# Kernel tuning notes

Measured on AMD Instinct MI355X. Metric: run time of the kernel, lower is better.

Reference implementation:

```python
import jax, jax.numpy as jnp
import numpy as np

N_HEADS = 16
HID_DIM = 64
INPUT_DIM = 1024
B, L = 4, 1024
NEG = -10000000000.0


def setup_inputs() -> dict:
    key = jax.random.key(0)
    ks = jax.random.split(key, 10)
    d = INPUT_DIM
    h = N_HEADS * HID_DIM
    s = 1.0 / np.sqrt(d)
    return {
        "query": jax.random.normal(ks[0], (B, L, d), dtype=jnp.float32),
        "key": jax.random.normal(ks[1], (B, L, d), dtype=jnp.float32),
        "value": jax.random.normal(ks[2], (B, L, d), dtype=jnp.float32),
        "mask": jax.random.randint(ks[3], (B, 1, L, L), 0, 2, dtype=jnp.int32),
        "wq": jax.random.normal(ks[4], (d, h), dtype=jnp.float32) * s,
        "bq": jnp.zeros((h,), dtype=jnp.float32),
        "wk": jax.random.normal(ks[5], (d, h), dtype=jnp.float32) * s,
        "bk": jnp.zeros((h,), dtype=jnp.float32),
        "wv": jax.random.normal(ks[6], (d, h), dtype=jnp.float32) * s,
        "bv": jnp.zeros((h,), dtype=jnp.float32),
    }


def _split_heads(x):
    # [B, L, H*D] -> [B, H, L, D]
    b, l, _ = x.shape
    return x.reshape(b, l, N_HEADS, HID_DIM).transpose(0, 2, 1, 3)


def reference(query, key, value, mask, wq, bq, wk, bk, wv, bv):
    scale = jnp.sqrt(jnp.float32(HID_DIM))
    Q = _split_heads(query @ wq + bq)   # [B,H,L,D]
    K = _split_heads(key @ wk + bk)
    V = _split_heads(value @ wv + bv)
    energy = jnp.einsum("bhqd,bhkd->bhqk", Q, K) / scale
    energy = jnp.where(mask == 0, jnp.float32(NEG), energy)
    attention = energy  # NOTE: softmax is intentionally skipped, as in the source
    x = jnp.einsum("bhqk,bhkd->bhqd", attention, V)
    x = x.transpose(0, 2, 1, 3).reshape(query.shape[0], -1, N_HEADS * HID_DIM)
    return (attention, x)
```

## Files before the change

kernel.cpp:

```cpp
#include <hip/hip_runtime.h>
#include <stdint.h>
#include <stddef.h>


typedef __attribute__((ext_vector_type(8))) short short8;
typedef __attribute__((ext_vector_type(4))) float f32x4;
typedef __attribute__((ext_vector_type(4))) int i32x4;
typedef __attribute__((ext_vector_type(2))) unsigned int u32x2;

#define MFMA16(a, b, c) __builtin_amdgcn_mfma_f32_16x16x32_bf16(a, b, c, 0, 0, 0)

using gptr_t = const __attribute__((address_space(1))) void*;
using lptr_t = __attribute__((address_space(3))) void*;

#define NEGV -10000000000.0f
#define NEGV_BF16 0xD015u

__device__ __forceinline__ unsigned short f2bf(float f) {
  uint32_t u = __builtin_bit_cast(uint32_t, f);
  u += 0x7FFFu + ((u >> 16) & 1u);
  return (unsigned short)(u >> 16);
}

__global__ __launch_bounds__(256) void k_convert(
    const float* __restrict__ q, const float* __restrict__ k, const float* __restrict__ v,
    unsigned short* __restrict__ oq, unsigned short* __restrict__ ok,
    unsigned short* __restrict__ ov) {
  const int z = blockIdx.z;
  const float* src = z == 0 ? q : z == 1 ? k : v;
  unsigned short* dst = z == 0 ? oq : z == 1 ? ok : ov;
  const size_t idx = ((size_t)blockIdx.x * 256 + threadIdx.x) * 8;
  f32x4 a = *(const f32x4*)(src + idx);
  f32x4 b = *(const f32x4*)(src + idx + 4);
  short8 o;
  o[0] = (short)f2bf(a[0]); o[1] = (short)f2bf(a[1]);
  o[2] = (short)f2bf(a[2]); o[3] = (short)f2bf(a[3]);
  o[4] = (short)f2bf(b[0]); o[5] = (short)f2bf(b[1]);
  o[6] = (short)f2bf(b[2]); o[7] = (short)f2bf(b[3]);
  *(short8*)(dst + idx) = o;
}

__global__ __launch_bounds__(256) void k_wt(
    const float* __restrict__ wq, const float* __restrict__ wk, const float* __restrict__ wv,
    unsigned short* __restrict__ tq, unsigned short* __restrict__ tk,
    unsigned short* __restrict__ tv) {
  const int z = blockIdx.z;
  const float* src = z == 0 ? wq : z == 1 ? wk : wv;
  unsigned short* dst = z == 0 ? tq : z == 1 ? tk : tv;
  __shared__ unsigned short t[64][65];
  const int n0 = blockIdx.x * 64, k0 = blockIdx.y * 64;
#pragma unroll
  for (int i = 0; i < 16; ++i) {
    const int idx = i * 256 + threadIdx.x;
    const int r = idx >> 6, c = idx & 63;
    t[r][c] = f2bf(src[(size_t)(k0 + r) * 1024 + n0 + c]);
  }
  __syncthreads();
#pragma unroll
  for (int i = 0; i < 16; ++i) {
    const int idx = i * 256 + threadIdx.x;
    const int r = idx >> 6, c = idx & 63;
    dst[(size_t)(n0 + r) * 1024 + k0 + c] = t[c][r];
  }
}

__global__ __launch_bounds__(256) void k_gemm(
    const unsigned short* __restrict__ Xq, const unsigned short* __restrict__ Xk,
    const unsigned short* __restrict__ Xv,
    const unsigned short* __restrict__ Wq, const unsigned short* __restrict__ Wk,
    const unsigned short* __restrict__ Wv,
    const float* __restrict__ bq, const float* __restrict__ bk, const float* __restrict__ bv,
    unsigned short* __restrict__ Cq, unsigned short* __restrict__ Ck,
    unsigned short* __restrict__ Vt) {
  const int bid = blockIdx.x;
  const int wg = (bid & 7) * 96 + (bid >> 3);
  const int z = wg >> 8, rem = wg & 255;
  const unsigned short* X  = z == 0 ? Xq : z == 1 ? Xk : Xv;
  const unsigned short* Wt = z == 0 ? Wq : z == 1 ? Wk : Wv;
  const float* bias        = z == 0 ? bq : z == 1 ? bk : bv;

  __shared__ unsigned short Ads[128 * 64];
  __shared__ unsigned short Bds[128 * 64];

  const int tid = threadIdx.x;
  const int w = tid >> 6, l = tid & 63;
  const int lr = l & 15, g = l >> 4;
  const int m0 = (rem >> 3) * 128, n0 = (rem & 7) * 128;
  const int wm = (w >> 1) * 64, wn = (w & 1) * 64;
  const int srow = tid >> 3, sslot = tid & 7;

  f32x4 acc[4][4];
#pragma unroll
  for (int mi = 0; mi < 4; ++mi)
#pragma unroll
    for (int ni = 0; ni < 4; ++ni) acc[mi][ni] = (f32x4){0.f, 0.f, 0.f, 0.f};

  for (int kt = 0; kt < 16; ++kt) {
    const int kb = kt * 64;
#pragma unroll
    for (int i = 0; i < 4; ++i) {
      const int row = i * 32 + srow;
      const int scol = ((sslot ^ (row & 7)) << 3);
      const unsigned short* ga = X + (size_t)(m0 + row) * 1024 + kb + scol;
      const unsigned short* gb = Wt + (size_t)(n0 + row) * 1024 + kb + scol;
      __builtin_amdgcn_global_load_lds((gptr_t)ga, (lptr_t)&Ads[(i * 32 + w * 8) * 64], 16, 0, 0);
      __builtin_amdgcn_global_load_lds((gptr_t)gb, (lptr_t)&Bds[(i * 32 + w * 8) * 64], 16, 0, 0);
    }
    __syncthreads();
    short8 afr[4][2], bfr[4][2];
#pragma unroll
    for (int t = 0; t < 4; ++t)
#pragma unroll
      for (int ks = 0; ks < 2; ++ks) {
        const int ra = wm + t * 16 + lr;
        afr[t][ks] = *(const short8*)&Ads[ra * 64 + (((ks * 4 + g) ^ (ra & 7)) << 3)];
        const int rb = wn + t * 16 + lr;
        bfr[t][ks] = *(const short8*)&Bds[rb * 64 + (((ks * 4 + g) ^ (rb & 7)) << 3)];
      }
#pragma unroll
    for (int ks = 0; ks < 2; ++ks)
#pragma unroll
      for (int mi = 0; mi < 4; ++mi)
#pragma unroll
        for (int ni = 0; ni < 4; ++ni)
          acc[mi][ni] = MFMA16(afr[mi][ks], bfr[ni][ks], acc[mi][ni]);
    __syncthreads();
  }

  if (z != 2) {
    unsigned short* C = z == 0 ? Cq : Ck;
#pragma unroll
    for (int mi = 0; mi < 4; ++mi)
#pragma unroll
      for (int ni = 0; ni < 4; ++ni) {
        const int n = n0 + wn + ni * 16 + lr;
        const float bs = bias[n];
        f32x4 a = acc[mi][ni];
#pragma unroll
        for (int r = 0; r < 4; ++r) {
          const int m = m0 + wm + mi * 16 + g * 4 + r;
          C[(size_t)m * 1024 + n] = f2bf(a[r] + bs);
        }
      }
  } else {
#pragma unroll
    for (int mi = 0; mi < 4; ++mi)
#pragma unroll
      for (int ni = 0; ni < 4; ++ni) {
        const int ng = n0 + wn + ni * 16 + lr;
        const int hh = ng >> 6, dd = ng & 63;
        const float bs = bias[ng];
        f32x4 a = acc[mi][ni];
        const int mg = m0 + wm + mi * 16 + g * 4;
        const int bb = mg >> 10, ll = mg & 1023;
        u32x2 pk;
        pk[0] = (uint32_t)f2bf(a[0] + bs) | ((uint32_t)f2bf(a[1] + bs) << 16);
        pk[1] = (uint32_t)f2bf(a[2] + bs) | ((uint32_t)f2bf(a[3] + bs) << 16);
        *(u32x2*)&Vt[(size_t)((bb * 16 + hh) * 64 + dd) * 1024 + ll] = pk;
      }
  }
}

__global__ __launch_bounds__(512, 4) void k_attn(
    const unsigned short* __restrict__ Qb, const unsigned short* __restrict__ Kb,
    const unsigned short* __restrict__ Vt, const int* __restrict__ mask,
    float* __restrict__ att, float* __restrict__ xout) {
  const int bid = blockIdx.x;
  const int wg = (bid & 7) * 64 + (bid >> 3);
  const int bh = wg >> 3, qt = wg & 7;
  const int b = bh >> 4, h = bh & 15;
  const int tid = threadIdx.x;
  const int w = tid >> 6, l = tid & 63;
  const int lr = l & 15, g = l >> 4;
  const int q0 = qt * 128 + w * 16;

  __shared__ unsigned short Kl[128 * 64];
  __shared__ unsigned short Vl[64 * 128];
  __shared__ unsigned short Pl[8 * 16 * 128];
  unsigned short* Pw = &Pl[w * 16 * 128];

  short8 qf[2];
#pragma unroll
  for (int ks = 0; ks < 2; ++ks)
    qf[ks] = *(const short8*)&Qb[(size_t)(b * 1024 + q0 + lr) * 1024 +
                                 h * 64 + ks * 32 + g * 8];

  f32x4 xacc[4];
#pragma unroll
  for (int di = 0; di < 4; ++di) xacc[di] = (f32x4){0.f, 0.f, 0.f, 0.f};

  for (int kt = 0; kt < 8; ++kt) {
    const int kb = kt * 128;
    __syncthreads();
#pragma unroll
    for (int i = 0; i < 2; ++i) {
      const int row = i * 64 + (tid >> 3);
      const int slot = tid & 7;
      const unsigned short* src = Kb + (size_t)(b * 1024 + kb + row) * 1024 +
                                  h * 64 + ((slot ^ (row & 7)) << 3);
      __builtin_amdgcn_global_load_lds((gptr_t)src, (lptr_t)&Kl[(i * 64 + w * 8) * 64], 16, 0, 0);
    }
#pragma unroll
    for (int i = 0; i < 2; ++i) {
      const int row = i * 32 + (tid >> 4);
      const int slot = tid & 15;
      const unsigned short* src = Vt + (size_t)(bh * 64 + row) * 1024 + kb +
                                  ((slot ^ (row & 7)) << 3);
      __builtin_amdgcn_global_load_lds((gptr_t)src, (lptr_t)&Vl[(i * 32 + w * 4) * 128], 16, 0, 0);
    }
    __syncthreads();

    f32x4 s[8];
#pragma unroll
    for (int ni = 0; ni < 8; ++ni) {
      f32x4 a = (f32x4){0.f, 0.f, 0.f, 0.f};
#pragma unroll
      for (int ks = 0; ks < 2; ++ks) {
        const int row = ni * 16 + lr;
        short8 kf = *(const short8*)&Kl[row * 64 + (((ks * 4 + g) ^ (row & 7)) << 3)];
        a = MFMA16(kf, qf[ks], a);
      }
      s[ni] = a;
    }
#pragma unroll
    for (int ni = 0; ni < 8; ++ni) {
      u32x2 pk;
      pk[0] = (uint32_t)f2bf(s[ni][0] * 0.125f) | ((uint32_t)f2bf(s[ni][1] * 0.125f) << 16);
      pk[1] = (uint32_t)f2bf(s[ni][2] * 0.125f) | ((uint32_t)f2bf(s[ni][3] * 0.125f) << 16);
      const int colq = ni * 16 + g * 4;
      *(u32x2*)&Pw[lr * 128 + (colq ^ ((lr & 7) << 3))] = pk;
    }
    asm volatile("s_waitcnt lgkmcnt(0)" ::: "memory");
    __builtin_amdgcn_sched_barrier(0);
#pragma unroll
    for (int p = 0; p < 8; ++p) {
      const int flat = p * 256 + l * 4;
      const int row = flat >> 7;
      const int col = flat & 127;
      const int eb = row * 128 + (col ^ ((row & 7) << 3));
      u32x2 pr = *(const u32x2*)&Pw[eb];
      i32x4 mv = *(const i32x4*)&mask[(size_t)(b * 1024 + q0 + row) * 1024 + kb + col];
      const uint32_t u0 = pr[0], u1 = pr[1];
      f32x4 e;
      e[0] = mv[0] ? __builtin_bit_cast(float, u0 << 16) : NEGV;
      e[1] = mv[1] ? __builtin_bit_cast(float, u0 & 0xFFFF0000u) : NEGV;
      e[2] = mv[2] ? __builtin_bit_cast(float, u1 << 16) : NEGV;
      e[3] = mv[3] ? __builtin_bit_cast(float, u1 & 0xFFFF0000u) : NEGV;
      __builtin_nontemporal_store(
          e, (f32x4*)&att[(size_t)(bh * 1024 + q0 + row) * 1024 + kb + col]);
      u32x2 wb;
      wb[0] = (mv[0] ? (u0 & 0xFFFFu) : NEGV_BF16) |
              ((mv[1] ? (u0 >> 16) : NEGV_BF16) << 16);
      wb[1] = (mv[2] ? (u1 & 0xFFFFu) : NEGV_BF16) |
              ((mv[3] ? (u1 >> 16) : NEGV_BF16) << 16);
      *(u32x2*)&Pw[eb] = wb;
    }
    asm volatile("s_waitcnt lgkmcnt(0)" ::: "memory");
    __builtin_amdgcn_sched_barrier(0);
#pragma unroll
    for (int ks4 = 0; ks4 < 4; ++ks4) {
      const int colk = ks4 * 32 + g * 8;
      short8 pa = *(const short8*)&Pw[lr * 128 + (colk ^ ((lr & 7) << 3))];
#pragma unroll
      for (int di = 0; di < 4; ++di) {
        const int vr = di * 16 + lr;
        short8 vf = *(const short8*)&Vl[vr * 128 + (colk ^ ((vr & 7) << 3))];
        xacc[di] = MFMA16(pa, vf, xacc[di]);
      }
    }
    asm volatile("" ::: "memory");
  }

#pragma unroll
  for (int di = 0; di < 4; ++di) {
    f32x4 a = xacc[di];
#pragma unroll
    for (int r = 0; r < 4; ++r) {
      const int q = q0 + g * 4 + r;
      __builtin_nontemporal_store(
          a[r], &xout[(size_t)(b * 1024 + q) * 1024 + h * 64 + di * 16 + lr]);
    }
  }
}

extern "C" void kernel_launch(void* const* d_in, const int* in_sizes, int n_in,
                              void* d_out, int out_size, void* d_ws, size_t ws_size,
                              hipStream_t stream) {
  (void)in_sizes; (void)n_in; (void)out_size;
  const float* q   = (const float*)d_in[0];
  const float* k   = (const float*)d_in[1];
  const float* v   = (const float*)d_in[2];
  const int* mask  = (const int*)d_in[3];
  const float* wq  = (const float*)d_in[4];
  const float* bq  = (const float*)d_in[5];
  const float* wk  = (const float*)d_in[6];
  const float* bk  = (const float*)d_in[7];
  const float* wv  = (const float*)d_in[8];
  const float* bv  = (const float*)d_in[9];
  float* att = (float*)d_out;
  float* x   = att + (size_t)4 * 16 * 1024 * 1024;

  char* ws = (char*)d_ws;
  const size_t SZX = (size_t)4096 * 1024 * 2;
  const size_t SZW = (size_t)1024 * 1024 * 2;
  if (ws_size < 6 * SZX + 3 * SZW) return;
  unsigned short* Xq  = (unsigned short*)(ws);
  unsigned short* Xk  = (unsigned short*)(ws + SZX);
  unsigned short* Xv  = (unsigned short*)(ws + 2 * SZX);
  unsigned short* Wtq = (unsigned short*)(ws + 3 * SZX);
  unsigned short* Wtk = (unsigned short*)(ws + 3 * SZX + SZW);
  unsigned short* Wtv = (unsigned short*)(ws + 3 * SZX + 2 * SZW);
  unsigned short* Qb  = (unsigned short*)(ws + 3 * SZX + 3 * SZW);
  unsigned short* Kb  = (unsigned short*)(ws + 4 * SZX + 3 * SZW);
  unsigned short* Vt  = (unsigned short*)(ws + 5 * SZX + 3 * SZW);

  k_convert<<<dim3(2048, 1, 3), 256, 0, stream>>>(q, k, v, Xq, Xk, Xv);
  k_wt<<<dim3(16, 16, 3), 256, 0, stream>>>(wq, wk, wv, Wtq, Wtk, Wtv);
  k_gemm<<<dim3(768), 256, 0, stream>>>(Xq, Xk, Xv, Wtq, Wtk, Wtv,
                                        bq, bk, bv, Qb, Kb, Vt);
  k_attn<<<dim3(512), 512, 0, stream>>>(Qb, Kb, Vt, mask, att, x);
}
```

Baseline: 147.7 us.

## Split attention tile into two 64-column halves to halve P scratch and raise occupancy

Each 128-key tile is now processed as two 64-key halves. Each half computes scores, applies the mask, writes the attention output and accumulates P·V, so the per-wave P scratch in LDS shrinks from 16x128 to 16x64. The swizzle is rewritten for the narrower rows. The launch-bounds occupancy hint rises from 4 to 6 blocks per CU, aiming to cut LDS and register pressure so more blocks fit per CU. The trade-off is more waitcnt/sched barriers per tile and shorter bursts of independent MFMA work between them.

```diff
diff --git a/kernel.cpp b/kernel.cpp
--- a/kernel.cpp
+++ b/kernel.cpp
@@ -161,7 +161,7 @@
   }
 }
 
-__global__ __launch_bounds__(512, 4) void k_attn(
+__global__ __launch_bounds__(512, 6) void k_attn(
     const unsigned short* __restrict__ Qb, const unsigned short* __restrict__ Kb,
     const unsigned short* __restrict__ Vt, const int* __restrict__ mask,
     float* __restrict__ att, float* __restrict__ xout) {
@@ -176,8 +176,8 @@
 
   __shared__ unsigned short Kl[128 * 64];
   __shared__ unsigned short Vl[64 * 128];
-  __shared__ unsigned short Pl[8 * 16 * 128];
-  unsigned short* Pw = &Pl[w * 16 * 128];
+  __shared__ unsigned short Pl[8][16 * 64];
+  unsigned short* Pw = Pl[w];
 
   short8 qf[2];
 #pragma unroll
@@ -210,65 +210,69 @@
     }
     __syncthreads();
 
-    f32x4 s[8];
-#pragma unroll
-    for (int ni = 0; ni < 8; ++ni) {
-      f32x4 a = (f32x4){0.f, 0.f, 0.f, 0.f};
-#pragma unroll
-      for (int ks = 0; ks < 2; ++ks) {
-        const int row = ni * 16 + lr;
-        short8 kf = *(const short8*)&Kl[row * 64 + (((ks * 4 + g) ^ (row & 7)) << 3)];
-        a = MFMA16(kf, qf[ks], a);
-      }
-      s[ni] = a;
-    }
-#pragma unroll
-    for (int ni = 0; ni < 8; ++ni) {
-      u32x2 pk;
-      pk[0] = (uint32_t)f2bf(s[ni][0] * 0.125f) | ((uint32_t)f2bf(s[ni][1] * 0.125f) << 16);
-      pk[1] = (uint32_t)f2bf(s[ni][2] * 0.125f) | ((uint32_t)f2bf(s[ni][3] * 0.125f) << 16);
-      const int colq = ni * 16 + g * 4;
-      *(u32x2*)&Pw[lr * 128 + (colq ^ ((lr & 7) << 3))] = pk;
-    }
-    asm volatile("s_waitcnt lgkmcnt(0)" ::: "memory");
-    __builtin_amdgcn_sched_barrier(0);
-#pragma unroll
-    for (int p = 0; p < 8; ++p) {
-      const int flat = p * 256 + l * 4;
-      const int row = flat >> 7;
-      const int col = flat & 127;
-      const int eb = row * 128 + (col ^ ((row & 7) << 3));
-      u32x2 pr = *(const u32x2*)&Pw[eb];
-      i32x4 mv = *(const i32x4*)&mask[(size_t)(b * 1024 + q0 + row) * 1024 + kb + col];
-      const uint32_t u0 = pr[0], u1 = pr[1];
-      f32x4 e;
-      e[0] = mv[0] ? __builtin_bit_cast(float, u0 << 16) : NEGV;
-      e[1] = mv[1] ? __builtin_bit_cast(float, u0 & 0xFFFF0000u) : NEGV;
-      e[2] = mv[2] ? __builtin_bit_cast(float, u1 << 16) : NEGV;
-      e[3] = mv[3] ? __builtin_bit_cast(float, u1 & 0xFFFF0000u) : NEGV;
-      __builtin_nontemporal_store(
-          e, (f32x4*)&att[(size_t)(bh * 1024 + q0 + row) * 1024 + kb + col]);
-      u32x2 wb;
-      wb[0] = (mv[0] ? (u0 & 0xFFFFu) : NEGV_BF16) |
-              ((mv[1] ? (u0 >> 16) : NEGV_BF16) << 16);
-      wb[1] = (mv[2] ? (u1 & 0xFFFFu) : NEGV_BF16) |
-              ((mv[3] ? (u1 >> 16) : NEGV_BF16) << 16);
-      *(u32x2*)&Pw[eb] = wb;
-    }
-    asm volatile("s_waitcnt lgkmcnt(0)" ::: "memory");
-    __builtin_amdgcn_sched_barrier(0);
-#pragma unroll
-    for (int ks4 = 0; ks4 < 4; ++ks4) {
-      const int colk = ks4 * 32 + g * 8;
-      short8 pa = *(const short8*)&Pw[lr * 128 + (colk ^ ((lr & 7) << 3))];
-#pragma unroll
-      for (int di = 0; di < 4; ++di) {
-        const int vr = di * 16 + lr;
-        short8 vf = *(const short8*)&Vl[vr * 128 + (colk ^ ((vr & 7) << 3))];
-        xacc[di] = MFMA16(pa, vf, xacc[di]);
-      }
-    }
-    asm volatile("" ::: "memory");
+#pragma unroll
+    for (int h2 = 0; h2 < 2; ++h2) {
+      f32x4 s[4];
+#pragma unroll
+      for (int n2 = 0; n2 < 4; ++n2) {
+        const int row = (h2 * 4 + n2) * 16 + lr;
+        f32x4 a = (f32x4){0.f, 0.f, 0.f, 0.f};
+#pragma unroll
+        for (int ks = 0; ks < 2; ++ks) {
+          short8 kf = *(const short8*)&Kl[row * 64 + (((ks * 4 + g) ^ (row & 7)) << 3)];
+          a = MFMA16(kf, qf[ks], a);
+        }
+        s[n2] = a;
+      }
+#pragma unroll
+      for (int n2 = 0; n2 < 4; ++n2) {
+        u32x2 pk;
+        pk[0] = (uint32_t)f2bf(s[n2][0] * 0.125f) | ((uint32_t)f2bf(s[n2][1] * 0.125f) << 16);
+        pk[1] = (uint32_t)f2bf(s[n2][2] * 0.125f) | ((uint32_t)f2bf(s[n2][3] * 0.125f) << 16);
+        const int c16 = n2 * 2 + (g >> 1);
+        *(u32x2*)&Pw[lr * 64 + ((c16 ^ (lr & 7)) << 3) + (g & 1) * 4] = pk;
+      }
+      asm volatile("s_waitcnt lgkmcnt(0)" ::: "memory");
+      __builtin_amdgcn_sched_barrier(0);
+#pragma unroll
+      for (int p = 0; p < 4; ++p) {
+        const int row = p * 4 + g;
+        const int col = lr * 4;
+        const int eb = row * 64 + (((lr >> 1) ^ (row & 7)) << 3) + (lr & 1) * 4;
+        u32x2 pr = *(const u32x2*)&Pw[eb];
+        i32x4 mv = *(const i32x4*)&mask[(size_t)(b * 1024 + q0 + row) * 1024 +
+                                        kb + h2 * 64 + col];
+        const uint32_t u0 = pr[0], u1 = pr[1];
+        f32x4 e;
+        e[0] = mv[0] ? __builtin_bit_cast(float, u0 << 16) : NEGV;
+        e[1] = mv[1] ? __builtin_bit_cast(float, u0 & 0xFFFF0000u) : NEGV;
+        e[2] = mv[2] ? __builtin_bit_cast(float, u1 << 16) : NEGV;
+        e[3] = mv[3] ? __builtin_bit_cast(float, u1 & 0xFFFF0000u) : NEGV;
+        __builtin_nontemporal_store(
+            e, (f32x4*)&att[(size_t)(bh * 1024 + q0 + row) * 1024 + kb + h2 * 64 + col]);
+        u32x2 wb;
+        wb[0] = (mv[0] ? (u0 & 0xFFFFu) : NEGV_BF16) |
+                ((mv[1] ? (u0 >> 16) : NEGV_BF16) << 16);
+        wb[1] = (mv[2] ? (u1 & 0xFFFFu) : NEGV_BF16) |
+                ((mv[3] ? (u1 >> 16) : NEGV_BF16) << 16);
+        *(u32x2*)&Pw[eb] = wb;
+      }
+      asm volatile("s_waitcnt lgkmcnt(0)" ::: "memory");
+      __builtin_amdgcn_sched_barrier(0);
+#pragma unroll
+      for (int k2 = 0; k2 < 2; ++k2) {
+        const int c16 = k2 * 4 + g;
+        short8 pa = *(const short8*)&Pw[lr * 64 + ((c16 ^ (lr & 7)) << 3)];
+        const int colk = h2 * 64 + k2 * 32 + g * 8;
+#pragma unroll
+        for (int di = 0; di < 4; ++di) {
+          const int vr = di * 16 + lr;
+          short8 vf = *(const short8*)&Vl[vr * 128 + (colk ^ ((vr & 7) << 3))];
+          xacc[di] = MFMA16(pa, vf, xacc[di]);
+        }
+      }
+      asm volatile("" ::: "memory");
+    }
   }
 
 #pragma unroll
```

New measurement: 164.1 us. 11.2% more time.
